# Optimization experiments

Hardware: AMD Instinct MI355X
Metric: run time of the kernel (lower is better)

The kernel has to match this reference:

```python
import jax, jax.numpy as jnp
import numpy as np

DIM = 1024


def setup_inputs() -> dict:
    key = jax.random.key(0)
    ks = jax.random.split(key, 10)
    B, S, D = 4, 2048, DIM
    std = 1.0 / np.sqrt(D)  # torch Linear default uniform bound
    return {
        "query": jax.random.normal(ks[0], (B, S, D), jnp.float32),
        "key": jax.random.normal(ks[1], (B, S, D), jnp.float32),
        "value": jax.random.normal(ks[2], (B, S, D), jnp.float32),
        "context": jnp.zeros((D,), jnp.float32),
        "Wq": jax.random.uniform(ks[3], (D, D), jnp.float32, -std, std),
        "bq": jax.random.uniform(ks[4], (D,), jnp.float32, -std, std),
        "Wk": jax.random.uniform(ks[5], (D, D), jnp.float32, -std, std),
        "bk": jax.random.uniform(ks[6], (D,), jnp.float32, -std, std),
        "Wv": jax.random.uniform(ks[7], (D, D), jnp.float32, -std, std),
        "bv": jax.random.uniform(ks[8], (D,), jnp.float32, -std, std),
    }


def reference(query, key, value, context, Wq, bq, Wk, bk, Wv, bv):
    scale = query.shape[-1] ** -0.5
    # torch Linear: x @ W.T + b
    q = (query + context) @ Wq.T + bq          # [B,S,D]
    k = (key + context) @ Wk.T + bk            # [B,S,D]
    v = value @ Wv.T + bv                      # [B,S,D]
    scores = jnp.einsum("bqd,bkd->bqk", q, k) * scale  # [B,S,S]
    weights = jax.nn.softmax(scores, axis=-1)
    return jnp.einsum("bqk,bkd->bqd", weights, v)
```

## Files before the change

### kernel.cpp

```cpp
#include <hip/hip_runtime.h>

typedef __attribute__((ext_vector_type(8))) short bf16x8;
typedef __attribute__((ext_vector_type(4))) float floatx4;

constexpr int BATCH = 4;
constexpr int SEQ   = 2048;
constexpr int DIMN  = 1024;
constexpr int M1    = BATCH * SEQ;

__device__ __forceinline__ short f2bf(float f) {
    union { float f; unsigned u; } x; x.f = f;
    unsigned r = x.u + 0x7fffu + ((x.u >> 16) & 1u);
    return (short)(r >> 16);
}
__device__ __forceinline__ float bf2f(short s) {
    union { unsigned u; float f; } x; x.u = ((unsigned)(unsigned short)s) << 16;
    return x.f;
}

__device__ __forceinline__ void async16(const void* g, void* l) {
    __builtin_amdgcn_global_load_lds(
        (const __attribute__((address_space(1))) unsigned int*)g,
        (__attribute__((address_space(3))) unsigned int*)l, 16, 0, 0);
}

#define WAITVM(N) asm volatile("s_waitcnt vmcnt(" #N ")" ::: "memory")
#define MEMFENCE  asm volatile("" ::: "memory")

template<bool OUT_BF16>
__device__ __forceinline__ void gemm256(
    const short* __restrict__ Ab, int lda,
    const short* __restrict__ Bb, int ldb,
    void* __restrict__ Cb, int ldc,
    const float* __restrict__ bias, int K, float scale,
    int m0, int n0)
{
    __shared__ alignas(16) char smem[3][49152];

    const int t    = threadIdx.x;
    const int lane = t & 63;
    const int wave = t >> 6;
    const int wr   = wave >> 2;
    const int wc   = wave & 3;
    const int lr   = lane & 15;
    const int lq   = lane >> 4;

    const short* pA[4];
    const short* pB[2];
    #pragma unroll
    for (int s = 0; s < 4; ++s) {
        const int P = s * 8192 + t * 16;
        const int L = P ^ (((P >> 7) & 7) << 4);
        pA[s] = Ab + (size_t)(m0 + (L >> 7)) * lda + ((L & 127) >> 1);
    }
    #pragma unroll
    for (int s = 0; s < 2; ++s) {
        const int P = s * 8192 + t * 16;
        const int L = P ^ (((P >> 7) & 7) << 4);
        pB[s] = Bb + (size_t)(n0 + (L >> 7)) * ldb + ((L & 127) >> 1);
    }

    int roA[8], roB[2], colp[2];
    #pragma unroll
    for (int m = 0; m < 8; ++m) roA[m] = (wr * 128 + m * 16 + lr) * 128;
    #pragma unroll
    for (int n = 0; n < 2; ++n) roB[n] = 32768 + (wc * 32 + n * 16 + lr) * 128;
    #pragma unroll
    for (int kk = 0; kk < 2; ++kk)
        colp[kk] = ((kk << 6) | (lq << 4)) ^ ((lane & 7) << 4);

    floatx4 acc[8][2];
    #pragma unroll
    for (int m = 0; m < 8; ++m)
        #pragma unroll
        for (int n = 0; n < 2; ++n) acc[m][n] = (floatx4)(0.f);

    const int ldst = t * 16;
    auto stage_a = [&](int sb) {
        char* base = smem[sb];
        async16(pA[0], base +          ldst);
        async16(pA[1], base +  8192 + ldst);
        async16(pA[2], base + 16384 + ldst);
        pA[0] += 64; pA[1] += 64; pA[2] += 64;
    };
    auto stage_b = [&](int sb) {
        char* base = smem[sb];
        async16(pA[3], base + 24576 + ldst);
        async16(pB[0], base + 32768 + ldst);
        async16(pB[1], base + 40960 + ldst);
        pA[3] += 64; pB[0] += 64; pB[1] += 64;
    };
    auto compute = [&](int buf, int kk) {
        const char* base = smem[buf];
        bf16x8 a[8], bfr[2];
        #pragma unroll
        for (int m = 0; m < 8; ++m)
            a[m] = *(const bf16x8*)(base + roA[m] + colp[kk]);
        #pragma unroll
        for (int n = 0; n < 2; ++n)
            bfr[n] = *(const bf16x8*)(base + roB[n] + colp[kk]);
        __builtin_amdgcn_s_setprio(1);
        #pragma unroll
        for (int m = 0; m < 8; ++m)
            #pragma unroll
            for (int n = 0; n < 2; ++n)
                acc[m][n] = __builtin_amdgcn_mfma_f32_16x16x32_bf16(
                    a[m], bfr[n], acc[m][n], 0, 0, 0);
        __builtin_amdgcn_s_setprio(0);
    };

    const int NT = K >> 6;
    stage_a(0); stage_b(0);
    stage_a(1); stage_b(1);

    int buf = 0;
    for (int tt = 0; tt < NT; ++tt) {
        const int  sb  = (buf == 0) ? 2 : buf - 1;
        const bool stg = (tt + 2) < NT;
        if (stg) stage_a(sb);
        if (tt + 2 < NT)      { WAITVM(9); }
        else if (tt + 1 < NT) { WAITVM(6); }
        else                  { WAITVM(0); }
        __builtin_amdgcn_s_barrier();
        MEMFENCE;
        compute(buf, 0);
        MEMFENCE;
        __builtin_amdgcn_s_barrier();
        if (stg) stage_b(sb);
        __builtin_amdgcn_s_barrier();
        MEMFENCE;
        compute(buf, 1);
        MEMFENCE;
        __builtin_amdgcn_s_barrier();
        buf = (buf == 2) ? 0 : buf + 1;
    }

    #pragma unroll
    for (int n = 0; n < 2; ++n) {
        const int gn = n0 + wc * 32 + n * 16 + lr;
        const float bv = bias ? bias[gn] : 0.f;
        #pragma unroll
        for (int m = 0; m < 8; ++m) {
            #pragma unroll
            for (int r = 0; r < 4; ++r) {
                const int gm = m0 + wr * 128 + m * 16 + lq * 4 + r;
                const float v = acc[m][n][r] * scale + bv;
                if (OUT_BF16) ((short*)Cb)[(size_t)gm * ldc + gn] = f2bf(v);
                else          ((float*)Cb)[(size_t)gm * ldc + gn] = v;
            }
        }
    }
}

__global__ __launch_bounds__(512)
void proj_qkv(const short* __restrict__ xq, const short* __restrict__ xk,
              const short* __restrict__ xv,
              const short* __restrict__ Wq_, const short* __restrict__ Wk_,
              const short* __restrict__ Wv_,
              const float* __restrict__ bq_, const float* __restrict__ bk_,
              const float* __restrict__ bv_,
              short* __restrict__ q, short* __restrict__ k, short* __restrict__ vp)
{
    const int b   = blockIdx.x;
    const int xcd = b & 7;
    const int i   = b >> 3;
    const int z   = i >> 5;
    const int r   = i & 31;
    const int mm  = r >> 3;
    const int nn  = r & 7;
    const short* X = (z == 0) ? xq : (z == 1) ? xk : xv;
    const short* W = (z == 0) ? Wq_ : (z == 1) ? Wk_ : Wv_;
    const float* bb = (z == 0) ? bq_ : (z == 1) ? bk_ : bv_;
    short* O = (z == 0) ? q : (z == 1) ? k : vp;
    gemm256<true>(X, DIMN, W, DIMN, (void*)O, DIMN, bb, DIMN, 1.f,
                  (xcd * 4 + mm) * 256, nn * 128);
}

__global__ __launch_bounds__(512)
void gemm_scores(const short* __restrict__ q, const short* __restrict__ k,
                 short* __restrict__ S, float scale)
{
    const int b   = blockIdx.x;
    const int xcd = b & 7;
    const int i   = b >> 3;
    const int bz  = xcd >> 1;
    const int mh  = xcd & 1;
    const int mm  = i >> 4;
    const int nn  = i & 15;
    gemm256<true>(q + (size_t)bz * SEQ * DIMN, DIMN,
                  k + (size_t)bz * SEQ * DIMN, DIMN,
                  (void*)(S + (size_t)bz * SEQ * SEQ), SEQ,
                  nullptr, DIMN, scale,
                  (mh * 4 + mm) * 256, nn * 128);
}

__global__ __launch_bounds__(512)
void gemm_pv(const short* __restrict__ P, const short* __restrict__ vt,
             float* __restrict__ O)
{
    const int b   = blockIdx.x;
    const int xcd = b & 7;
    const int i   = b >> 3;
    const int bz  = xcd >> 1;
    const int mh  = xcd & 1;
    const int mm  = i >> 3;
    const int nn  = i & 7;
    gemm256<false>(P  + (size_t)bz * SEQ * SEQ,  SEQ,
                   vt + (size_t)bz * DIMN * SEQ, SEQ,
                   (void*)(O + (size_t)bz * SEQ * DIMN), DIMN,
                   nullptr, SEQ, 1.f,
                   (mh * 4 + mm) * 256, nn * 128);
}

__global__ __launch_bounds__(256)
void cvt_tri(const float* __restrict__ in0, short* __restrict__ out0,
             const float* __restrict__ in1, short* __restrict__ out1,
             const float* __restrict__ in2, short* __restrict__ out2, int n8)
{
    const int z = blockIdx.z;
    const float* in = (z == 0) ? in0 : (z == 1) ? in1 : in2;
    short* out      = (z == 0) ? out0 : (z == 1) ? out1 : out2;
    const int i = blockIdx.x * 256 + threadIdx.x;
    if (i >= n8) return;
    const float4 a0 = ((const float4*)in)[(size_t)i * 2];
    const float4 a1 = ((const float4*)in)[(size_t)i * 2 + 1];
    const float v[8] = {a0.x, a0.y, a0.z, a0.w, a1.x, a1.y, a1.z, a1.w};
    bf16x8 o;
    #pragma unroll
    for (int j = 0; j < 8; ++j) o[j] = f2bf(v[j]);
    *(bf16x8*)(out + (size_t)i * 8) = o;
}

__global__ __launch_bounds__(256)
void bias3(const float* __restrict__ Wq, const float* __restrict__ Wk,
           const float* __restrict__ Wv,
           const float* __restrict__ bq, const float* __restrict__ bk,
           const float* __restrict__ bv,
           const float* __restrict__ ctx,
           float* __restrict__ oq, float* __restrict__ ok, float* __restrict__ ov)
{
    const int z = blockIdx.y;
    const float* W = (z == 0) ? Wq : (z == 1) ? Wk : Wv;
    const float* b = (z == 0) ? bq : (z == 1) ? bk : bv;
    float*       o = (z == 0) ? oq : (z == 1) ? ok : ov;
    const int n    = blockIdx.x * 4 + (threadIdx.x >> 6);
    const int lane = threadIdx.x & 63;
    float s = 0.f;
    if (z < 2) {
        const float* row = W + (size_t)n * DIMN;
        for (int k = lane * 4; k < DIMN; k += 256) {
            const float4 x = *(const float4*)(row + k);
            const float4 c = *(const float4*)(ctx + k);
            s += x.x * c.x + x.y * c.y + x.z * c.z + x.w * c.w;
        }
        #pragma unroll
        for (int off = 32; off > 0; off >>= 1) s += __shfl_xor(s, off);
    }
    if (lane == 0) o[n] = b[n] + s;
}

__global__ __launch_bounds__(256)
void transpose_v(const short* __restrict__ in, short* __restrict__ out)
{
    __shared__ short t[64][68];
    const int b  = blockIdx.z;
    const int d0 = blockIdx.x * 64;
    const int s0 = blockIdx.y * 64;
    const int r  = threadIdx.x >> 3;
    const int c  = (threadIdx.x & 7) * 8;
    #pragma unroll
    for (int h = 0; h < 2; ++h) {
        const int s = r + h * 32;
        bf16x8 v = *(const bf16x8*)(in + ((size_t)b * SEQ + s0 + s) * DIMN + d0 + c);
        #pragma unroll
        for (int j = 0; j < 8; ++j) t[c + j][s] = v[j];
    }
    __syncthreads();
    #pragma unroll
    for (int h = 0; h < 2; ++h) {
        const int d = r + h * 32;
        bf16x8 v;
        #pragma unroll
        for (int j = 0; j < 8; ++j) v[j] = t[d][c + j];
        *(bf16x8*)(out + ((size_t)b * DIMN + d0 + d) * SEQ + s0 + c) = v;
    }
}

__global__ __launch_bounds__(256)
void softmax_kernel(short* __restrict__ P)
{
    const int bid = blockIdx.x;
    const int xcd = bid & 7;
    const int i   = bid >> 3;
    const int row = (xcd >> 1) * SEQ + (xcd & 1) * 1024 + i;
    short* p = P + (size_t)row * SEQ;
    const int t    = threadIdx.x;
    const int lane = t & 63;
    const int wave = t >> 6;
    __shared__ float red[8];

    bf16x8 raw = *(const bf16x8*)(p + t * 8);
    float v[8];
    float mx = -1e30f;
    #pragma unroll
    for (int j = 0; j < 8; ++j) { v[j] = bf2f(raw[j]); mx = fmaxf(mx, v[j]); }
    #pragma unroll
    for (int off = 32; off > 0; off >>= 1) mx = fmaxf(mx, __shfl_xor(mx, off));
    if (lane == 0) red[wave] = mx;
    __syncthreads();
    mx = fmaxf(fmaxf(red[0], red[1]), fmaxf(red[2], red[3]));

    float e[8], s = 0.f;
    #pragma unroll
    for (int j = 0; j < 8; ++j) { e[j] = __expf(v[j] - mx); s += e[j]; }
    #pragma unroll
    for (int off = 32; off > 0; off >>= 1) s += __shfl_xor(s, off);
    if (lane == 0) red[4 + wave] = s;
    __syncthreads();
    s = red[4] + red[5] + red[6] + red[7];
    const float inv = 1.f / s;

    bf16x8 o;
    #pragma unroll
    for (int j = 0; j < 8; ++j) o[j] = f2bf(e[j] * inv);
    *(bf16x8*)(p + t * 8) = o;
}

extern "C" void kernel_launch(void* const* d_in, const int* in_sizes, int n_in,
                              void* d_out, int out_size, void* d_ws, size_t ws_size,
                              hipStream_t stream)
{
    const float* query = (const float*)d_in[0];
    const float* key_  = (const float*)d_in[1];
    const float* value = (const float*)d_in[2];
    const float* ctx   = (const float*)d_in[3];
    const float* Wq    = (const float*)d_in[4];
    const float* bq    = (const float*)d_in[5];
    const float* Wk    = (const float*)d_in[6];
    const float* bk    = (const float*)d_in[7];
    const float* Wv    = (const float*)d_in[8];
    const float* bv    = (const float*)d_in[9];

    char* ws = (char*)d_ws;
    char* od = (char*)d_out;
    const size_t MB = 1ull << 20;
    short* xq   = (short*)(ws);
    short* xk   = (short*)(ws + 16 * MB);
    short* q_b  = (short*)(ws + 32 * MB);
    short* k_b  = (short*)(ws + 48 * MB);
    short* Wq_b = (short*)(ws + 64 * MB);
    short* Wk_b = (short*)(ws + 66 * MB);
    short* Wv_b = (short*)(ws + 68 * MB);
    float* bq_e = (float*)(ws + 70 * MB);
    float* bk_e = (float*)(ws + 70 * MB + 4096);
    float* bv_e = (float*)(ws + 70 * MB + 8192);
    short* S_b  = (short*)(ws);
    short* v_t  = (short*)(ws + 64 * MB);
    short* xv   = (short*)(od);
    short* vp   = (short*)(od + 16 * MB);

    dim3 blk(256);
    dim3 blk512(512);
    const int W8 = DIMN * DIMN / 8;
    const int X8 = M1 * DIMN / 8;

    cvt_tri<<<dim3(W8 / 256, 1, 3), blk, 0, stream>>>(Wq, Wq_b, Wk, Wk_b, Wv, Wv_b, W8);
    bias3<<<dim3(DIMN / 4, 3), blk, 0, stream>>>(Wq, Wk, Wv, bq, bk, bv, ctx,
                                                 bq_e, bk_e, bv_e);
    cvt_tri<<<dim3(X8 / 256, 1, 3), blk, 0, stream>>>(query, xq, key_, xk, value, xv, X8);

    proj_qkv<<<dim3(768), blk512, 0, stream>>>(xq, xk, xv, Wq_b, Wk_b, Wv_b,
                                               bq_e, bk_e, bv_e, q_b, k_b, vp);
    transpose_v<<<dim3(DIMN / 64, SEQ / 64, BATCH), blk, 0, stream>>>(vp, v_t);

    const float scale = 1.0f / 32.0f;
    gemm_scores<<<dim3(512), blk512, 0, stream>>>(q_b, k_b, S_b, scale);

    softmax_kernel<<<dim3(M1), blk, 0, stream>>>(S_b);

    gemm_pv<<<dim3(256), blk512, 0, stream>>>(S_b, v_t, (float*)d_out);
}
```

Baseline: 320.4 us.

## Rework GEMM core with double-buffered LDS, wider N tiles and templated M tile

Replaces the three-stage 256x128 GEMM pipeline with a two-buffer LDS pipeline. The new kernel uses 256-wide N tiles, a templated M tile (256 for scores, 128 for the projection and PV GEMMs) and finer interleaving of async loads with MFMA phases. The scores grid is halved to 256 blocks and launch bounds ask for two blocks per CU. The aim is more operand reuse per LDS load and better occupancy and load overlap. In exchange there are more barriers per K step and more register pressure from the 8x4 accumulator tile.

```diff
diff --git a/kernel.cpp b/kernel.cpp
--- a/kernel.cpp
+++ b/kernel.cpp
@@ -26,16 +26,22 @@
 
 #define WAITVM(N) asm volatile("s_waitcnt vmcnt(" #N ")" ::: "memory")
 #define MEMFENCE  asm volatile("" ::: "memory")
-
-template<bool OUT_BF16>
-__device__ __forceinline__ void gemm256(
+#define BAR()     __builtin_amdgcn_s_barrier()
+#define PRIO(x)   __builtin_amdgcn_s_setprio(x)
+
+template<bool OUT_BF16, int WM>
+__device__ __forceinline__ void gemm_core(
     const short* __restrict__ Ab, int lda,
     const short* __restrict__ Bb, int ldb,
     void* __restrict__ Cb, int ldc,
     const float* __restrict__ bias, int K, float scale,
     int m0, int n0)
 {
-    __shared__ alignas(16) char smem[3][49152];
+    constexpr int ACH  = WM / 2;
+    constexpr int ABY  = WM * 4096;
+    constexpr int BUFB = ABY + 32768;
+    __shared__ alignas(16) char smem[2][BUFB];
+    char* lds = &smem[0][0];
 
     const int t    = threadIdx.x;
     const int lane = t & 63;
@@ -45,105 +51,168 @@
     const int lr   = lane & 15;
     const int lq   = lane >> 4;
 
-    const short* pA[4];
-    const short* pB[2];
-    #pragma unroll
-    for (int s = 0; s < 4; ++s) {
-        const int P = s * 8192 + t * 16;
-        const int L = P ^ (((P >> 7) & 7) << 4);
-        pA[s] = Ab + (size_t)(m0 + (L >> 7)) * lda + ((L & 127) >> 1);
+    const int srow = t >> 3;
+    const int scol = (((t & 7) * 16) ^ (((t >> 3) & 7) << 4)) >> 1;
+    const short* pa = Ab + (size_t)(m0 + srow) * lda + scol;
+    const short* pb = Bb + (size_t)(n0 + srow) * ldb + scol;
+    const size_t rsa = (size_t)64 * lda;
+    const size_t rsb = (size_t)64 * ldb;
+    const int ldst = t * 16;
+
+    const int roA0 = (wr * (WM * 16) + lr) * 128;
+    const int roB0 = ABY + (wc * 64 + lr) * 128;
+    const int cp0  = (lq << 4) ^ ((lane & 7) << 4);
+
+    floatx4 acc[WM][4];
+    #pragma unroll
+    for (int m = 0; m < WM; ++m)
+        #pragma unroll
+        for (int n = 0; n < 4; ++n) acc[m][n] = (floatx4)(0.f);
+
+    auto stA = [&](int dstb) {
+        #pragma unroll
+        for (int c = 0; c < ACH; ++c)
+            async16(pa + (size_t)c * rsa, lds + dstb + c * 8192 + ldst);
+        pa += 64;
+    };
+    auto stB01 = [&](int dstb) {
+        async16(pb,       lds + dstb + ABY +        ldst);
+        async16(pb + rsb, lds + dstb + ABY + 8192 + ldst);
+    };
+    auto stB23 = [&](int dstb) {
+        async16(pb + 2 * rsb, lds + dstb + ABY + 16384 + ldst);
+        async16(pb + 3 * rsb, lds + dstb + ABY + 24576 + ldst);
+        pb += 64;
+    };
+
+    const int NT = K >> 6;
+
+    stA(0); stB01(0); stB23(0); stA(BUFB);
+    if constexpr (WM == 8) WAITVM(4); else WAITVM(2);
+    BAR();
+
+    for (int tt = 0; tt < NT; tt += 2) {
+        #pragma unroll
+        for (int half = 0; half < 2; ++half) {
+            const int bufb = half ? BUFB : 0;
+            const int tc   = tt + half;
+            const char* rb = lds + bufb;
+
+            if constexpr (WM == 8) {
+                bf16x8 af[8], bq_[4];
+                #pragma unroll
+                for (int m = 0; m < 8; ++m)
+                    af[m] = *(const bf16x8*)(rb + roA0 + m * 2048 + cp0);
+                bq_[0] = *(const bf16x8*)(rb + roB0 +        cp0);
+                bq_[1] = *(const bf16x8*)(rb + roB0 + 2048 + cp0);
+                if (tc + 1 < NT) stB01(bufb ^ BUFB);
+                BAR(); MEMFENCE;
+                PRIO(1);
+                #pragma unroll
+                for (int m = 0; m < 8; ++m) {
+                    acc[m][0] = __builtin_amdgcn_mfma_f32_16x16x32_bf16(af[m], bq_[0], acc[m][0], 0, 0, 0);
+                    acc[m][1] = __builtin_amdgcn_mfma_f32_16x16x32_bf16(af[m], bq_[1], acc[m][1], 0, 0, 0);
+                }
+                PRIO(0);
+                MEMFENCE; BAR();
+                bq_[2] = *(const bf16x8*)(rb + roB0 + 2 * 2048 + cp0);
+                bq_[3] = *(const bf16x8*)(rb + roB0 + 3 * 2048 + cp0);
+                if (tc + 1 < NT) stB23(bufb ^ BUFB);
+                BAR(); MEMFENCE;
+                PRIO(1);
+                #pragma unroll
+                for (int m = 0; m < 8; ++m) {
+                    acc[m][2] = __builtin_amdgcn_mfma_f32_16x16x32_bf16(af[m], bq_[2], acc[m][2], 0, 0, 0);
+                    acc[m][3] = __builtin_amdgcn_mfma_f32_16x16x32_bf16(af[m], bq_[3], acc[m][3], 0, 0, 0);
+                }
+                PRIO(0);
+                MEMFENCE; BAR();
+                #pragma unroll
+                for (int m = 0; m < 8; ++m)
+                    af[m] = *(const bf16x8*)(rb + roA0 + m * 2048 + (cp0 ^ 64));
+                bq_[0] = *(const bf16x8*)(rb + roB0 +        (cp0 ^ 64));
+                bq_[1] = *(const bf16x8*)(rb + roB0 + 2048 + (cp0 ^ 64));
+                BAR(); MEMFENCE;
+                PRIO(1);
+                #pragma unroll
+                for (int m = 0; m < 8; ++m) {
+                    acc[m][0] = __builtin_amdgcn_mfma_f32_16x16x32_bf16(af[m], bq_[0], acc[m][0], 0, 0, 0);
+                    acc[m][1] = __builtin_amdgcn_mfma_f32_16x16x32_bf16(af[m], bq_[1], acc[m][1], 0, 0, 0);
+                }
+                PRIO(0);
+                MEMFENCE; BAR();
+                bq_[2] = *(const bf16x8*)(rb + roB0 + 2 * 2048 + (cp0 ^ 64));
+                bq_[3] = *(const bf16x8*)(rb + roB0 + 3 * 2048 + (cp0 ^ 64));
+                if (tc + 2 < NT) stA(bufb);
+                BAR(); MEMFENCE;
+                PRIO(1);
+                #pragma unroll
+                for (int m = 0; m < 8; ++m) {
+                    acc[m][2] = __builtin_amdgcn_mfma_f32_16x16x32_bf16(af[m], bq_[2], acc[m][2], 0, 0, 0);
+                    acc[m][3] = __builtin_amdgcn_mfma_f32_16x16x32_bf16(af[m], bq_[3], acc[m][3], 0, 0, 0);
+                }
+                PRIO(0);
+                MEMFENCE;
+                if (tc + 2 < NT)      { WAITVM(4); }
+                else if (tc + 1 < NT) { WAITVM(0); }
+                BAR();
+            } else {
+                bf16x8 af[4][2], bq_[2][2];
+                #pragma unroll
+                for (int m = 0; m < 4; ++m) {
+                    af[m][0] = *(const bf16x8*)(rb + roA0 + m * 2048 + cp0);
+                    af[m][1] = *(const bf16x8*)(rb + roA0 + m * 2048 + (cp0 ^ 64));
+                }
+                #pragma unroll
+                for (int n = 0; n < 2; ++n) {
+                    bq_[n][0] = *(const bf16x8*)(rb + roB0 + n * 2048 + cp0);
+                    bq_[n][1] = *(const bf16x8*)(rb + roB0 + n * 2048 + (cp0 ^ 64));
+                }
+                if (tc + 1 < NT) { stB01(bufb ^ BUFB); stB23(bufb ^ BUFB); }
+                BAR(); MEMFENCE;
+                PRIO(1);
+                #pragma unroll
+                for (int m = 0; m < 4; ++m)
+                    #pragma unroll
+                    for (int n = 0; n < 2; ++n) {
+                        acc[m][n] = __builtin_amdgcn_mfma_f32_16x16x32_bf16(af[m][0], bq_[n][0], acc[m][n], 0, 0, 0);
+                        acc[m][n] = __builtin_amdgcn_mfma_f32_16x16x32_bf16(af[m][1], bq_[n][1], acc[m][n], 0, 0, 0);
+                    }
+                PRIO(0);
+                MEMFENCE; BAR();
+                #pragma unroll
+                for (int n = 0; n < 2; ++n) {
+                    bq_[n][0] = *(const bf16x8*)(rb + roB0 + (n + 2) * 2048 + cp0);
+                    bq_[n][1] = *(const bf16x8*)(rb + roB0 + (n + 2) * 2048 + (cp0 ^ 64));
+                }
+                if (tc + 2 < NT) stA(bufb);
+                BAR(); MEMFENCE;
+                PRIO(1);
+                #pragma unroll
+                for (int m = 0; m < 4; ++m)
+                    #pragma unroll
+                    for (int n = 0; n < 2; ++n) {
+                        acc[m][n + 2] = __builtin_amdgcn_mfma_f32_16x16x32_bf16(af[m][0], bq_[n][0], acc[m][n + 2], 0, 0, 0);
+                        acc[m][n + 2] = __builtin_amdgcn_mfma_f32_16x16x32_bf16(af[m][1], bq_[n][1], acc[m][n + 2], 0, 0, 0);
+                    }
+                PRIO(0);
+                MEMFENCE;
+                if (tc + 2 < NT)      { WAITVM(2); }
+                else if (tc + 1 < NT) { WAITVM(0); }
+                BAR();
+            }
+        }
     }
-    #pragma unroll
-    for (int s = 0; s < 2; ++s) {
-        const int P = s * 8192 + t * 16;
-        const int L = P ^ (((P >> 7) & 7) << 4);
-        pB[s] = Bb + (size_t)(n0 + (L >> 7)) * ldb + ((L & 127) >> 1);
-    }
-
-    int roA[8], roB[2], colp[2];
-    #pragma unroll
-    for (int m = 0; m < 8; ++m) roA[m] = (wr * 128 + m * 16 + lr) * 128;
-    #pragma unroll
-    for (int n = 0; n < 2; ++n) roB[n] = 32768 + (wc * 32 + n * 16 + lr) * 128;
-    #pragma unroll
-    for (int kk = 0; kk < 2; ++kk)
-        colp[kk] = ((kk << 6) | (lq << 4)) ^ ((lane & 7) << 4);
-
-    floatx4 acc[8][2];
-    #pragma unroll
-    for (int m = 0; m < 8; ++m)
-        #pragma unroll
-        for (int n = 0; n < 2; ++n) acc[m][n] = (floatx4)(0.f);
-
-    const int ldst = t * 16;
-    auto stage_a = [&](int sb) {
-        char* base = smem[sb];
-        async16(pA[0], base +          ldst);
-        async16(pA[1], base +  8192 + ldst);
-        async16(pA[2], base + 16384 + ldst);
-        pA[0] += 64; pA[1] += 64; pA[2] += 64;
-    };
-    auto stage_b = [&](int sb) {
-        char* base = smem[sb];
-        async16(pA[3], base + 24576 + ldst);
-        async16(pB[0], base + 32768 + ldst);
-        async16(pB[1], base + 40960 + ldst);
-        pA[3] += 64; pB[0] += 64; pB[1] += 64;
-    };
-    auto compute = [&](int buf, int kk) {
-        const char* base = smem[buf];
-        bf16x8 a[8], bfr[2];
-        #pragma unroll
-        for (int m = 0; m < 8; ++m)
-            a[m] = *(const bf16x8*)(base + roA[m] + colp[kk]);
-        #pragma unroll
-        for (int n = 0; n < 2; ++n)
-            bfr[n] = *(const bf16x8*)(base + roB[n] + colp[kk]);
-        __builtin_amdgcn_s_setprio(1);
-        #pragma unroll
-        for (int m = 0; m < 8; ++m)
-            #pragma unroll
-            for (int n = 0; n < 2; ++n)
-                acc[m][n] = __builtin_amdgcn_mfma_f32_16x16x32_bf16(
-                    a[m], bfr[n], acc[m][n], 0, 0, 0);
-        __builtin_amdgcn_s_setprio(0);
-    };
-
-    const int NT = K >> 6;
-    stage_a(0); stage_b(0);
-    stage_a(1); stage_b(1);
-
-    int buf = 0;
-    for (int tt = 0; tt < NT; ++tt) {
-        const int  sb  = (buf == 0) ? 2 : buf - 1;
-        const bool stg = (tt + 2) < NT;
-        if (stg) stage_a(sb);
-        if (tt + 2 < NT)      { WAITVM(9); }
-        else if (tt + 1 < NT) { WAITVM(6); }
-        else                  { WAITVM(0); }
-        __builtin_amdgcn_s_barrier();
-        MEMFENCE;
-        compute(buf, 0);
-        MEMFENCE;
-        __builtin_amdgcn_s_barrier();
-        if (stg) stage_b(sb);
-        __builtin_amdgcn_s_barrier();
-        MEMFENCE;
-        compute(buf, 1);
-        MEMFENCE;
-        __builtin_amdgcn_s_barrier();
-        buf = (buf == 2) ? 0 : buf + 1;
-    }
-
-    #pragma unroll
-    for (int n = 0; n < 2; ++n) {
-        const int gn = n0 + wc * 32 + n * 16 + lr;
+
+    #pragma unroll
+    for (int n = 0; n < 4; ++n) {
+        const int gn = n0 + wc * 64 + n * 16 + lr;
         const float bv = bias ? bias[gn] : 0.f;
         #pragma unroll
-        for (int m = 0; m < 8; ++m) {
+        for (int m = 0; m < WM; ++m) {
             #pragma unroll
             for (int r = 0; r < 4; ++r) {
-                const int gm = m0 + wr * 128 + m * 16 + lq * 4 + r;
+                const int gm = m0 + wr * (WM * 16) + m * 16 + lq * 4 + r;
                 const float v = acc[m][n][r] * scale + bv;
                 if (OUT_BF16) ((short*)Cb)[(size_t)gm * ldc + gn] = f2bf(v);
                 else          ((float*)Cb)[(size_t)gm * ldc + gn] = v;
@@ -152,7 +221,7 @@
     }
 }
 
-__global__ __launch_bounds__(512)
+__global__ __launch_bounds__(512, 2)
 void proj_qkv(const short* __restrict__ xq, const short* __restrict__ xk,
               const short* __restrict__ xv,
               const short* __restrict__ Wq_, const short* __restrict__ Wk_,
@@ -166,37 +235,19 @@
     const int i   = b >> 3;
     const int z   = i >> 5;
     const int r   = i & 31;
-    const int mm  = r >> 3;
-    const int nn  = r & 7;
+    const int mm  = r >> 2;
+    const int nn  = r & 3;
     const short* X = (z == 0) ? xq : (z == 1) ? xk : xv;
     const short* W = (z == 0) ? Wq_ : (z == 1) ? Wk_ : Wv_;
     const float* bb = (z == 0) ? bq_ : (z == 1) ? bk_ : bv_;
     short* O = (z == 0) ? q : (z == 1) ? k : vp;
-    gemm256<true>(X, DIMN, W, DIMN, (void*)O, DIMN, bb, DIMN, 1.f,
-                  (xcd * 4 + mm) * 256, nn * 128);
-}
-
-__global__ __launch_bounds__(512)
+    gemm_core<true, 4>(X, DIMN, W, DIMN, (void*)O, DIMN, bb, DIMN, 1.f,
+                       (xcd * 8 + mm) * 128, nn * 256);
+}
+
+__global__ __launch_bounds__(512, 2)
 void gemm_scores(const short* __restrict__ q, const short* __restrict__ k,
                  short* __restrict__ S, float scale)
-{
-    const int b   = blockIdx.x;
-    const int xcd = b & 7;
-    const int i   = b >> 3;
-    const int bz  = xcd >> 1;
-    const int mh  = xcd & 1;
-    const int mm  = i >> 4;
-    const int nn  = i & 15;
-    gemm256<true>(q + (size_t)bz * SEQ * DIMN, DIMN,
-                  k + (size_t)bz * SEQ * DIMN, DIMN,
-                  (void*)(S + (size_t)bz * SEQ * SEQ), SEQ,
-                  nullptr, DIMN, scale,
-                  (mh * 4 + mm) * 256, nn * 128);
-}
-
-__global__ __launch_bounds__(512)
-void gemm_pv(const short* __restrict__ P, const short* __restrict__ vt,
-             float* __restrict__ O)
 {
     const int b   = blockIdx.x;
     const int xcd = b & 7;
@@ -205,11 +256,29 @@
     const int mh  = xcd & 1;
     const int mm  = i >> 3;
     const int nn  = i & 7;
-    gemm256<false>(P  + (size_t)bz * SEQ * SEQ,  SEQ,
-                   vt + (size_t)bz * DIMN * SEQ, SEQ,
-                   (void*)(O + (size_t)bz * SEQ * DIMN), DIMN,
-                   nullptr, SEQ, 1.f,
-                   (mh * 4 + mm) * 256, nn * 128);
+    gemm_core<true, 8>(q + (size_t)bz * SEQ * DIMN, DIMN,
+                       k + (size_t)bz * SEQ * DIMN, DIMN,
+                       (void*)(S + (size_t)bz * SEQ * SEQ), SEQ,
+                       nullptr, DIMN, scale,
+                       (mh * 4 + mm) * 256, nn * 256);
+}
+
+__global__ __launch_bounds__(512, 2)
+void gemm_pv(const short* __restrict__ P, const short* __restrict__ vt,
+             float* __restrict__ O)
+{
+    const int b   = blockIdx.x;
+    const int xcd = b & 7;
+    const int i   = b >> 3;
+    const int bz  = xcd >> 1;
+    const int mh  = xcd & 1;
+    const int mm  = i >> 2;
+    const int nn  = i & 3;
+    gemm_core<false, 4>(P  + (size_t)bz * SEQ * SEQ,  SEQ,
+                        vt + (size_t)bz * DIMN * SEQ, SEQ,
+                        (void*)(O + (size_t)bz * SEQ * DIMN), DIMN,
+                        nullptr, SEQ, 1.f,
+                        (mh * 8 + mm) * 128, nn * 256);
 }
 
 __global__ __launch_bounds__(256)
@@ -374,7 +443,7 @@
     transpose_v<<<dim3(DIMN / 64, SEQ / 64, BATCH), blk, 0, stream>>>(vp, v_t);
 
     const float scale = 1.0f / 32.0f;
-    gemm_scores<<<dim3(512), blk512, 0, stream>>>(q_b, k_b, S_b, scale);
+    gemm_scores<<<dim3(256), blk512, 0, stream>>>(q_b, k_b, S_b, scale);
 
     softmax_kernel<<<dim3(M1), blk, 0, stream>>>(S_b);
 
```

After: 304.3 us. 1.05x faster.
